# Optimization experiments

Hardware: AMD Instinct MI355X
Metric: run time of the kernel (lower is better)

## Reference

```python
import jax, jax.numpy as jnp
import numpy as np

SMALL_NUM = 0.015
B, R, F, H, A = 262144, 3, 4, 16, 18  # batch, rules, features-per-rule, hidden, action_dim


def setup_inputs() -> dict:
    key = jax.random.key(0)
    ks = jax.random.split(key, 10)
    s = jax.random.normal(ks[0], (B, F), dtype=jnp.float32)
    # membership-network params, stacked over (rule, feature); xavier-uniform-ish scales
    W1 = jax.random.uniform(ks[1], (R, F, H), minval=-1.0, maxval=1.0) * np.sqrt(6.0 / (1 + H))
    b1 = jnp.zeros((R, F, H), jnp.float32)
    W2 = jax.random.uniform(ks[2], (R, F, H, H), minval=-1.0, maxval=1.0) * np.sqrt(6.0 / (2 * H))
    b2 = jnp.zeros((R, F, H), jnp.float32)
    W3 = jax.random.uniform(ks[3], (R, F, H), minval=-1.0, maxval=1.0) * np.sqrt(6.0 / (H + 1))
    b3 = jnp.zeros((R, F), jnp.float32)
    # p_select init per Rule.__init__: column 0 = 0, column 1 = 10
    p_select = jnp.concatenate([jnp.zeros((R, F, 1)), jnp.full((R, F, 1), 10.0)], axis=-1).astype(jnp.float32)
    leaves_params = jax.random.normal(ks[4], (4, A), dtype=jnp.float32)
    # Gumbel(0,1) noise, drawn once (the torch module samples inside forward)
    U = jax.random.uniform(ks[5], (R, F, 2), minval=1e-6, maxval=1.0)
    gumbel_noise = -jnp.log(-jnp.log(U + 1e-20) + 1e-20)
    return {"s": s, "W1": W1, "b1": b1, "W2": W2, "b2": b2, "W3": W3, "b3": b3,
            "p_select": p_select, "leaves_params": leaves_params, "gumbel_noise": gumbel_noise}


def reference(s, W1, b1, W2, b2, W3, b3, p_select, leaves_params, gumbel_noise):
    lrelu = lambda x: jnp.where(x > 0, x, 0.01 * x)  # F.leaky_relu default slope
    # all 12 tiny MLPs (3 rules x 4 features) vectorized; input is the scalar feature s[:, f]
    h1 = lrelu(jnp.einsum('bf,rfh->brfh', s, W1) + b1)            # [B,R,F,H]
    h2 = lrelu(jnp.einsum('brfh,rfho->brfo', h1, W2) + b2)        # [B,R,F,H]
    m = jax.nn.sigmoid(jnp.einsum('brfh,rfh->brf', h2, W3) + b3)  # [B,R,F] membership
    m = jnp.maximum(m, SMALL_NUM)  # torch.where(m < SMALL, SMALL, m)
    # hard gumbel-softmax over last dim (torch dim=1 of a [F,2] tensor), straight-through
    y_soft = jax.nn.softmax(p_select + gumbel_noise, axis=-1)     # [R,F,2]
    y_hard = (y_soft == y_soft.max(-1, keepdims=True)).astype(y_soft.dtype)
    gs = jax.lax.stop_gradient(y_hard - y_soft) + y_soft
    gs1 = gs[..., 1]                                              # [R,F]
    soft_weight = gs1[None] / m                                   # [B,R,F]
    X_exp = jnp.exp(soft_weight * 0.1)
    cond = gs1.sum(-1) > SMALL_NUM                                # [R] per-rule masked softmax
    X_exp = jnp.where(cond[None, :, None], X_exp * gs1[None], X_exp)
    soft = X_exp / X_exp.sum(-1, keepdims=True)
    strength = (m * soft * gs1[None]).sum(-1)                     # [B,R]
    strength = jnp.where(jnp.isnan(strength), 0.0, strength)
    r0, r1, r2 = strength[:, 0:1], strength[:, 1:2], strength[:, 2:3]
    path_p = jnp.concatenate([r0 * r1, r0 * (1 - r1), (1 - r0) * r2, (1 - r0) * (1 - r2)], axis=1)  # [B,4]
    idx = jnp.argmax(path_p, axis=1)
    leaves_distribution = jax.nn.softmax(leaves_params, axis=1)   # [4,A]
    return leaves_distribution[idx]                               # [B,A]
```

## Files before the change

### kernel.cpp

```cpp
#include <hip/hip_runtime.h>
#include <math.h>

#define BTOT 262144
#define R 3
#define F 4
#define H 16
#define A 18
#define SMALL_NUM_F 0.015f

__global__ __launch_bounds__(256) void ftc_kernel(
    const float* __restrict__ s,
    const float* __restrict__ W1,
    const float* __restrict__ b1,
    const float* __restrict__ W2,
    const float* __restrict__ b2,
    const float* __restrict__ W3,
    const float* __restrict__ b3,
    const float* __restrict__ p_select,
    const float* __restrict__ leaves,
    const float* __restrict__ gumbel,
    float* __restrict__ out)
{
    __shared__ float sh_g[R][F];
    __shared__ float sh_cond[R];
    __shared__ float sh_leaves[4][A];
    __shared__ unsigned char sh_idx[256];

    const int tid = threadIdx.x;

    if (tid < R * F) {
        const int rf = tid;
        float l0 = p_select[rf * 2 + 0] + gumbel[rf * 2 + 0];
        float l1 = p_select[rf * 2 + 1] + gumbel[rf * 2 + 1];
        float mx = fmaxf(l0, l1);
        float e0 = expf(l0 - mx), e1 = expf(l1 - mx);
        float den = e0 + e1;
        float y0 = e0 / den, y1 = e1 / den;
        float ym = fmaxf(y0, y1);
        sh_g[rf / F][rf % F] = (y1 == ym) ? 1.0f : 0.0f;
    }
    if (tid < 4) {
        float mx = leaves[tid * A];
        for (int a = 1; a < A; ++a) mx = fmaxf(mx, leaves[tid * A + a]);
        float e[A];
        float sum = 0.f;
        for (int a = 0; a < A; ++a) { e[a] = expf(leaves[tid * A + a] - mx); sum += e[a]; }
        for (int a = 0; a < A; ++a) sh_leaves[tid][a] = e[a] / sum;
    }
    __syncthreads();
    if (tid < R) {
        float ssum = sh_g[tid][0] + sh_g[tid][1] + sh_g[tid][2] + sh_g[tid][3];
        sh_cond[tid] = (ssum > SMALL_NUM_F) ? 1.0f : 0.0f;
    }
    __syncthreads();

    const int b = blockIdx.x * 256 + tid;
    const float4 sv = *reinterpret_cast<const float4*>(s + (size_t)b * F);
    const float sf[F] = {sv.x, sv.y, sv.z, sv.w};

    float strength[R];
#pragma unroll
    for (int r = 0; r < R; ++r) {
        float m[F];
#pragma unroll
        for (int f = 0; f < F; ++f) {
            const int rf = r * F + f;
            const float* w1  = W1 + rf * H;
            const float* bb1 = b1 + rf * H;
            const float* w2  = W2 + rf * H * H;
            const float* bb2 = b2 + rf * H;
            const float* w3  = W3 + rf * H;

            float h1[H];
#pragma unroll
            for (int h = 0; h < H; ++h) {
                float v = fmaf(sf[f], w1[h], bb1[h]);
                h1[h] = fmaxf(v, 0.01f * v);
            }
            float acc[H];
#pragma unroll
            for (int o = 0; o < H; ++o) acc[o] = bb2[o];
#pragma unroll
            for (int h = 0; h < H; ++h) {
                const float hv = h1[h];
#pragma unroll
                for (int o = 0; o < H; ++o)
                    acc[o] = fmaf(hv, w2[h * H + o], acc[o]);
            }
            float dot = b3[rf];
#pragma unroll
            for (int o = 0; o < H; ++o) {
                float v = fmaxf(acc[o], 0.01f * acc[o]);
                dot = fmaf(v, w3[o], dot);
            }
            float mm = 1.0f / (1.0f + expf(-dot));
            m[f] = fmaxf(mm, SMALL_NUM_F);
        }

        const bool c = sh_cond[r] != 0.0f;
        float X[F];
        float ssum = 0.f;
#pragma unroll
        for (int f = 0; f < F; ++f) {
            float g = sh_g[r][f];
            float xw = expf(0.1f * (g / m[f]));
            if (c) xw *= g;
            X[f] = xw;
            ssum += xw;
        }
        float st = 0.f;
#pragma unroll
        for (int f = 0; f < F; ++f)
            st += m[f] * (X[f] / ssum) * sh_g[r][f];
        strength[r] = isnan(st) ? 0.0f : st;
    }

    const float r0 = strength[0], r1 = strength[1], r2 = strength[2];
    const float p0 = r0 * r1;
    const float p1 = r0 * (1.0f - r1);
    const float p2 = (1.0f - r0) * r2;
    const float p3 = (1.0f - r0) * (1.0f - r2);
    int idx = 0;
    float best = p0;
    if (p1 > best) { best = p1; idx = 1; }
    if (p2 > best) { best = p2; idx = 2; }
    if (p3 > best) { best = p3; idx = 3; }
    sh_idx[tid] = (unsigned char)idx;
    __syncthreads();

    float* outb = out + (size_t)blockIdx.x * (256 * A);
    for (int i = tid; i < 256 * A; i += 256) {
        int bl = i / A;
        int a  = i - bl * A;
        outb[i] = sh_leaves[sh_idx[bl]][a];
    }
}

extern "C" void kernel_launch(void* const* d_in, const int* in_sizes, int n_in,
                              void* d_out, int out_size, void* d_ws, size_t ws_size,
                              hipStream_t stream) {
    const float* s  = (const float*)d_in[0];
    const float* W1 = (const float*)d_in[1];
    const float* b1 = (const float*)d_in[2];
    const float* W2 = (const float*)d_in[3];
    const float* b2 = (const float*)d_in[4];
    const float* W3 = (const float*)d_in[5];
    const float* b3 = (const float*)d_in[6];
    const float* ps = (const float*)d_in[7];
    const float* lv = (const float*)d_in[8];
    const float* gn = (const float*)d_in[9];
    float* out = (float*)d_out;

    dim3 grid(BTOT / 256);
    dim3 block(256);
    hipLaunchKernelGGL(ftc_kernel, grid, block, 0, stream,
                       s, W1, b1, W2, b2, W3, b3, ps, lv, gn, out);
}
```

Baseline: 46.75 us.

## Collapse zero-bias membership MLPs into piecewise-linear slopes with exact fallback

A one-block setup kernel checks at runtime whether all first- and second-layer biases are zero. If they are, it precomputes, per rule and feature, the two effective slopes of the positively homogeneous leaky-ReLU MLP, one for positive input and one for negative. The main kernel then gets each membership logit with a single FMA instead of about 300 FMAs per tiny MLP. It falls back to the full exact MLP when biases are nonzero or when the top two path probabilities are within a small margin, so the argmax stays robust to rounding. The cost is an extra kernel launch, and any wavefront with one near-tie lane still runs the exact path for that whole wavefront.

```diff
diff --git a/kernel.cpp b/kernel.cpp
--- a/kernel.cpp
+++ b/kernel.cpp
@@ -7,6 +7,119 @@
 #define H 16
 #define A 18
 #define SMALL_NUM_F 0.015f
+#define MARGIN_TAU 3e-4f
+
+__global__ __launch_bounds__(192) void ftc_setup(
+    const float* __restrict__ W1,
+    const float* __restrict__ b1,
+    const float* __restrict__ W2,
+    const float* __restrict__ b2,
+    const float* __restrict__ W3,
+    float* __restrict__ ws)
+{
+    __shared__ int nz;
+    const int tid = threadIdx.x;
+    if (tid == 0) nz = 0;
+    __syncthreads();
+    if (tid < R * F * H) {
+        if (b1[tid] != 0.0f) atomicOr(&nz, 1);
+        if (b2[tid] != 0.0f) atomicOr(&nz, 1);
+    }
+    __syncthreads();
+    if (tid == 0) ((int*)ws)[0] = (nz == 0) ? 1 : 0;
+
+    if (tid < R * F) {
+        const int rf = tid;
+        double Kp = 0.0, Km = 0.0;
+        for (int o = 0; o < H; ++o) {
+            double Pp = 0.0, Pm = 0.0;
+            for (int h = 0; h < H; ++h) {
+                const double w1 = (double)W1[rf * H + h];
+                const double w2 = (double)W2[rf * H * H + h * H + o];
+                Pp += w1 * ((w1 > 0.0) ? 1.0 : 0.01) * w2;
+                Pm += w1 * ((w1 < 0.0) ? 1.0 : 0.01) * w2;
+            }
+            const double w3 = (double)W3[rf * H + o];
+            Kp += Pp * ((Pp > 0.0) ? 1.0 : 0.01) * w3;
+            Km += Pm * ((Pm < 0.0) ? 1.0 : 0.01) * w3;
+        }
+        ws[4 + rf]  = (float)Kp;
+        ws[20 + rf] = (float)Km;
+    }
+}
+
+__device__ __forceinline__ void compute_m_exact(
+    const float sf[F],
+    const float* __restrict__ W1, const float* __restrict__ b1,
+    const float* __restrict__ W2, const float* __restrict__ b2,
+    const float* __restrict__ W3, const float* __restrict__ b3,
+    float m[R][F])
+{
+#pragma unroll
+    for (int r = 0; r < R; ++r) {
+#pragma unroll
+        for (int f = 0; f < F; ++f) {
+            const int rf = r * F + f;
+            const float* w1  = W1 + rf * H;
+            const float* bb1 = b1 + rf * H;
+            const float* w2  = W2 + rf * H * H;
+            const float* bb2 = b2 + rf * H;
+            const float* w3  = W3 + rf * H;
+
+            float h1[H];
+#pragma unroll
+            for (int h = 0; h < H; ++h) {
+                float v = fmaf(sf[f], w1[h], bb1[h]);
+                h1[h] = fmaxf(v, 0.01f * v);
+            }
+            float acc[H];
+#pragma unroll
+            for (int o = 0; o < H; ++o) acc[o] = bb2[o];
+#pragma unroll
+            for (int h = 0; h < H; ++h) {
+                const float hv = h1[h];
+#pragma unroll
+                for (int o = 0; o < H; ++o)
+                    acc[o] = fmaf(hv, w2[h * H + o], acc[o]);
+            }
+            float dot = b3[rf];
+#pragma unroll
+            for (int o = 0; o < H; ++o) {
+                float v = fmaxf(acc[o], 0.01f * acc[o]);
+                dot = fmaf(v, w3[o], dot);
+            }
+            float mm = 1.0f / (1.0f + expf(-dot));
+            m[r][f] = fmaxf(mm, SMALL_NUM_F);
+        }
+    }
+}
+
+__device__ __forceinline__ void compute_strength(
+    const float m[R][F],
+    const float shg[R][F],
+    const float shcond[R],
+    float st[R])
+{
+#pragma unroll
+    for (int r = 0; r < R; ++r) {
+        const bool c = shcond[r] != 0.0f;
+        float X[F];
+        float ssum = 0.f;
+#pragma unroll
+        for (int f = 0; f < F; ++f) {
+            float g = shg[r][f];
+            float xw = expf(0.1f * (g / m[r][f]));
+            if (c) xw *= g;
+            X[f] = xw;
+            ssum += xw;
+        }
+        float sv = 0.f;
+#pragma unroll
+        for (int f = 0; f < F; ++f)
+            sv += m[r][f] * (X[f] / ssum) * shg[r][f];
+        st[r] = isnan(sv) ? 0.0f : sv;
+    }
+}
 
 __global__ __launch_bounds__(256) void ftc_kernel(
     const float* __restrict__ s,
@@ -19,6 +132,7 @@
     const float* __restrict__ p_select,
     const float* __restrict__ leaves,
     const float* __restrict__ gumbel,
+    const float* __restrict__ ws,
     float* __restrict__ out)
 {
     __shared__ float sh_g[R][F];
@@ -58,64 +172,49 @@
     const float4 sv = *reinterpret_cast<const float4*>(s + (size_t)b * F);
     const float sf[F] = {sv.x, sv.y, sv.z, sv.w};
 
-    float strength[R];
-#pragma unroll
-    for (int r = 0; r < R; ++r) {
-        float m[F];
-#pragma unroll
-        for (int f = 0; f < F; ++f) {
-            const int rf = r * F + f;
-            const float* w1  = W1 + rf * H;
-            const float* bb1 = b1 + rf * H;
-            const float* w2  = W2 + rf * H * H;
-            const float* bb2 = b2 + rf * H;
-            const float* w3  = W3 + rf * H;
-
-            float h1[H];
-#pragma unroll
-            for (int h = 0; h < H; ++h) {
-                float v = fmaf(sf[f], w1[h], bb1[h]);
-                h1[h] = fmaxf(v, 0.01f * v);
-            }
-            float acc[H];
-#pragma unroll
-            for (int o = 0; o < H; ++o) acc[o] = bb2[o];
-#pragma unroll
-            for (int h = 0; h < H; ++h) {
-                const float hv = h1[h];
-#pragma unroll
-                for (int o = 0; o < H; ++o)
-                    acc[o] = fmaf(hv, w2[h * H + o], acc[o]);
-            }
-            float dot = b3[rf];
-#pragma unroll
-            for (int o = 0; o < H; ++o) {
-                float v = fmaxf(acc[o], 0.01f * acc[o]);
-                dot = fmaf(v, w3[o], dot);
-            }
-            float mm = 1.0f / (1.0f + expf(-dot));
-            m[f] = fmaxf(mm, SMALL_NUM_F);
-        }
-
-        const bool c = sh_cond[r] != 0.0f;
-        float X[F];
-        float ssum = 0.f;
-#pragma unroll
-        for (int f = 0; f < F; ++f) {
-            float g = sh_g[r][f];
-            float xw = expf(0.1f * (g / m[f]));
-            if (c) xw *= g;
-            X[f] = xw;
-            ssum += xw;
-        }
-        float st = 0.f;
-#pragma unroll
-        for (int f = 0; f < F; ++f)
-            st += m[f] * (X[f] / ssum) * sh_g[r][f];
-        strength[r] = isnan(st) ? 0.0f : st;
-    }
-
-    const float r0 = strength[0], r1 = strength[1], r2 = strength[2];
+    const int flag = ((const int*)ws)[0];
+
+    float m[R][F];
+    float st[R];
+    bool need_exact = (flag == 0);
+
+    if (flag) {
+#pragma unroll
+        for (int r = 0; r < R; ++r) {
+#pragma unroll
+            for (int f = 0; f < F; ++f) {
+                const int rf = r * F + f;
+                const float kp = ws[4 + rf];
+                const float km = ws[20 + rf];
+                const float k = (sf[f] > 0.0f) ? kp : km;
+                const float dot = fmaf(sf[f], k, b3[rf]);
+                const float mm = 1.0f / (1.0f + expf(-dot));
+                m[r][f] = fmaxf(mm, SMALL_NUM_F);
+            }
+        }
+        compute_strength(m, sh_g, sh_cond, st);
+        {
+            const float r0 = st[0], r1 = st[1], r2 = st[2];
+            const float p0 = r0 * r1;
+            const float p1 = r0 * (1.0f - r1);
+            const float p2 = (1.0f - r0) * r2;
+            const float p3 = (1.0f - r0) * (1.0f - r2);
+            const float a = fmaxf(p0, p1), bb = fminf(p0, p1);
+            const float c = fmaxf(p2, p3), d = fminf(p2, p3);
+            const float best = fmaxf(a, c);
+            const float second = fmaxf(fminf(a, c), (a >= c) ? bb : d);
+            const float margin = best - second;
+            need_exact = !(margin > MARGIN_TAU);
+        }
+    }
+
+    if (need_exact) {
+        compute_m_exact(sf, W1, b1, W2, b2, W3, b3, m);
+    }
+
+    compute_strength(m, sh_g, sh_cond, st);
+
+    const float r0 = st[0], r1 = st[1], r2 = st[2];
     const float p0 = r0 * r1;
     const float p1 = r0 * (1.0f - r1);
     const float p2 = (1.0f - r0) * r2;
@@ -149,10 +248,11 @@
     const float* ps = (const float*)d_in[7];
     const float* lv = (const float*)d_in[8];
     const float* gn = (const float*)d_in[9];
+    float* ws  = (float*)d_ws;
     float* out = (float*)d_out;
 
-    dim3 grid(BTOT / 256);
-    dim3 block(256);
-    hipLaunchKernelGGL(ftc_kernel, grid, block, 0, stream,
-                       s, W1, b1, W2, b2, W3, b3, ps, lv, gn, out);
-}
+    hipLaunchKernelGGL(ftc_setup, dim3(1), dim3(192), 0, stream,
+                       W1, b1, W2, b2, W3, ws);
+    hipLaunchKernelGGL(ftc_kernel, dim3(BTOT / 256), dim3(256), 0, stream,
+                       s, W1, b1, W2, b2, W3, b3, ps, lv, gn, ws, out);
+}
```

Measured after the change: 63.03 us. 34.8% more time.
